# Optimization experiments

Hardware: AMD Instinct MI355X
Metric: run time of the kernel (lower is better)

The kernel has to match this reference:

```python
import jax, jax.numpy as jnp
import numpy as np
import math

B, S, HID = 1, 2048, 4096
NH, NKV, HD = 32, 8, 128
GROUPS = NH // NKV
THETA = 10000.0
NEG_INF = -1e9


def _ste(x, q):
    # straight-through estimator: forward uses q, backward passes grad to x
    return x + jax.lax.stop_gradient(q - x)


def fq_per_token(x):
    # symmetric int8 fake-quant, dynamic per-token scale over last dim
    s = jnp.maximum(jnp.max(jnp.abs(x), axis=-1, keepdims=True), 1e-8) / 127.0
    q = jnp.clip(jnp.round(x / s), -128.0, 127.0) * s
    return _ste(x, q)


def fq_per_channel(x):
    # symmetric int8 fake-quant, per-(head, channel) scale for K/V [B,H,S,D]
    s = jnp.maximum(jnp.max(jnp.abs(x), axis=(0, 2), keepdims=True), 1e-8) / 127.0
    q = jnp.clip(jnp.round(x / s), -128.0, 127.0) * s
    return _ste(x, q)


def _rotate_half(x):
    x1, x2 = jnp.split(x, 2, axis=-1)
    return jnp.concatenate([-x2, x1], axis=-1)


def _rope(position_ids):
    inv_freq = 1.0 / (THETA ** (jnp.arange(0, HD, 2, dtype=jnp.float32) / HD))
    freqs = position_ids.astype(jnp.float32)[..., None] * inv_freq  # [B,S,HD/2]
    emb = jnp.concatenate([freqs, freqs], axis=-1)                  # [B,S,HD]
    return jnp.cos(emb)[:, None, :, :], jnp.sin(emb)[:, None, :, :]


def setup_inputs() -> dict:
    key = jax.random.key(0)
    ks = jax.random.split(key, 9)
    w = 0.02
    return {
        "hidden_states": jax.random.normal(ks[0], (B, S, HID), dtype=jnp.float32),
        "position_ids": jnp.arange(B * S, dtype=jnp.int64 if jax.config.jax_enable_x64 else jnp.int32).reshape(B, S) % S,
        "Wq": jax.random.normal(ks[1], (HID, HID), dtype=jnp.float32) * w,
        "Wk": jax.random.normal(ks[2], (NKV * HD, HID), dtype=jnp.float32) * w,
        "Wv": jax.random.normal(ks[3], (NKV * HD, HID), dtype=jnp.float32) * w,
        "Wo": jax.random.normal(ks[4], (HID, HID), dtype=jnp.float32) * w,
        "qbias1": jax.random.normal(ks[5], (HID,), dtype=jnp.float32) * 0.01,
        "qbias2": jax.random.normal(ks[6], (HID,), dtype=jnp.float32) * 0.01,
        "o_scale2": jnp.ones((HID,), dtype=jnp.float32),
    }


def reference(hidden_states, position_ids, Wq, Wk, Wv, Wo, qbias1, qbias2, o_scale2):
    dtype = hidden_states.dtype
    # --- input activation quantization fused with qbias1 ---
    hs = fq_per_token(hidden_states - qbias1) + qbias1

    q = (hs @ Wq.T).reshape(B, S, NH, HD).transpose(0, 2, 1, 3)   # [B,NH,S,D]
    k = (hs @ Wk.T).reshape(B, S, NKV, HD).transpose(0, 2, 1, 3)  # [B,NKV,S,D]
    v = (hs @ Wv.T).reshape(B, S, NKV, HD).transpose(0, 2, 1, 3)

    cos, sin = _rope(position_ids)
    q = q * cos + _rotate_half(q) * sin
    k = k * cos + _rotate_half(k) * sin

    # repeat_kv for GQA
    k = jnp.repeat(k, GROUPS, axis=1)  # [B,NH,S,D]
    v = jnp.repeat(v, GROUPS, axis=1)

    # --- quantized QK^T ---
    k = fq_per_channel(k)          # qkt_matmul.quant_x2
    qq = fq_per_token(q)           # qkt_matmul quantizes x1
    attn = jnp.einsum("bhqd,bhkd->bhqk", qq, k) / math.sqrt(HD)

    # causal mask
    causal = jnp.tril(jnp.ones((S, S), dtype=bool))
    attn = jnp.where(causal[None, None], attn, jnp.asarray(NEG_INF, attn.dtype))

    attn = jax.nn.softmax(attn.astype(jnp.float32), axis=-1).astype(dtype)

    # --- quantized PV ---
    v = fq_per_channel(v)          # pv_matmul.quant_x2
    p = fq_per_token(attn)         # pv_matmul quantizes x1
    out = jnp.einsum("bhqk,bhkd->bhqd", p, v)
    out = fq_per_token(out)        # out_quant=True

    out = out.transpose(0, 2, 1, 3).reshape(B, S, HID)
    out = out * o_scale2
    # output activation quantization fused with qbias2
    out = fq_per_token(out - qbias2) + qbias2
    return out @ Wo.T
```

## Files before the change

kernel.cpp:

```cpp
#include <hip/hip_runtime.h>
#include <stdint.h>

typedef _Float16 f16;
typedef __bf16 bf16;
typedef f16 f16x4 __attribute__((ext_vector_type(4)));
typedef f16 f16x8 __attribute__((ext_vector_type(8)));
typedef bf16 bf16x4 __attribute__((ext_vector_type(4)));
typedef bf16 bf16x8 __attribute__((ext_vector_type(8)));
typedef float f32x4 __attribute__((ext_vector_type(4)));

#define SEQ 2048
#define HID 4096
#define NH 32
#define NKV 8
#define HD 128
#define NQKV 6144

__device__ __forceinline__ float fq_round(float x, float s){
  float r = rintf(x / s);
  r = fminf(fmaxf(r, -128.f), 127.f);
  return r * s;
}

__device__ __forceinline__ void gload_lds16(const void* g, void* l){
  __builtin_amdgcn_global_load_lds(
      (const __attribute__((address_space(1))) uint32_t*)g,
      (__attribute__((address_space(3))) uint32_t*)l, 16, 0, 0);
}

__device__ __forceinline__ void stage_g8(const void* gbase, size_t row_bytes, void* lds, int tid){
  int w = tid >> 6, l = tid & 63;
  #pragma unroll
  for (int i = 0; i < 4; i++){
    int flat = i * 256 + w * 64 + l;
    int r = flat >> 3, g = flat & 7;
    const char* src = (const char*)gbase + (size_t)r * row_bytes + (size_t)((g ^ (r & 7)) << 4);
    char* dst = (char*)lds + (size_t)(i * 256 + w * 64) * 16;
    gload_lds16(src, dst);
  }
}
__device__ __forceinline__ void stage_g16(const void* gbase, size_t row_bytes, void* lds, int tid){
  int w = tid >> 6, l = tid & 63;
  #pragma unroll
  for (int i = 0; i < 4; i++){
    int flat = i * 256 + w * 64 + l;
    int r = flat >> 4, g = flat & 15;
    const char* src = (const char*)gbase + (size_t)r * row_bytes + (size_t)((g ^ (r & 15)) << 4);
    char* dst = (char*)lds + (size_t)(i * 256 + w * 64) * 16;
    gload_lds16(src, dst);
  }
}

__global__ __launch_bounds__(256) void cvt_bf16_k(const float* __restrict__ x, bf16* __restrict__ y, int n4){
  int i = blockIdx.x * 256 + threadIdx.x;
  if (i < n4){
    float4 v = ((const float4*)x)[i];
    bf16x4 o = { (bf16)v.x, (bf16)v.y, (bf16)v.z, (bf16)v.w };
    ((bf16x4*)y)[i] = o;
  }
}

__global__ __launch_bounds__(256) void rope_table_k(const int* __restrict__ pos, float* __restrict__ cosT, float* __restrict__ sinT){
  int idx = blockIdx.x * 256 + threadIdx.x;
  int t = idx >> 6, j = idx & 63;
  float inv = powf(10000.f, -(float)j * (1.f/64.f));
  float f = (float)pos[t] * inv;
  cosT[idx] = cosf(f);
  sinT[idx] = sinf(f);
}

__global__ __launch_bounds__(256) void fq_hs_k(const float* __restrict__ h, const float* __restrict__ qb1, bf16* __restrict__ hs){
  int t = blockIdx.x, tid = threadIdx.x;
  const float* row = h + (size_t)t * HID;
  float x[16];
  float amax = 0.f;
  #pragma unroll
  for (int i = 0; i < 16; i++){
    int c = tid + i * 256;
    float v = row[c] - qb1[c];
    x[i] = v;
    amax = fmaxf(amax, fabsf(v));
  }
  #pragma unroll
  for (int d = 1; d < 64; d <<= 1) amax = fmaxf(amax, __shfl_xor(amax, d));
  __shared__ float red[4];
  if ((tid & 63) == 0) red[tid >> 6] = amax;
  __syncthreads();
  amax = fmaxf(fmaxf(red[0], red[1]), fmaxf(red[2], red[3]));
  float s = fmaxf(amax, 1e-8f) / 127.f;
  #pragma unroll
  for (int i = 0; i < 16; i++){
    int c = tid + i * 256;
    float q = fq_round(x[i], s) + qb1[c];
    hs[(size_t)t * HID + c] = (bf16)q;
  }
}

__global__ __launch_bounds__(512, 2) void gemm8(const bf16* __restrict__ A, const bf16* __restrict__ B,
                                                float* __restrict__ C, int N, int K){
  __shared__ bf16 As[2][256 * 64];
  __shared__ bf16 Bs[2][192 * 64];
  int orig = blockIdx.y * gridDim.x + blockIdx.x;
  int nid = (orig & 7) * 32 + (orig >> 3);
  int bm = (nid >> 5) * 256, bn = (nid & 31) * 192;
  int tid = threadIdx.x, lane = tid & 63, wid = tid >> 6;
  int wr = wid >> 2, wc = wid & 3;
  int lq = lane & 15, lg = lane >> 4;
  f32x4 acc[8][3] = {};
  int nk = K >> 6;

  const bf16* Abase = A + (size_t)bm * K;
  const bf16* Bbase = B + (size_t)bn * K;
  size_t rowb = (size_t)K * 2;

  auto stage_a = [&](bf16* lds, int t){
    const char* g0 = (const char*)Abase + (size_t)t * 128;
    #pragma unroll
    for (int i = 0; i < 4; i++){
      int f = i * 512 + tid;
      int r = f >> 3, g = f & 7;
      gload_lds16(g0 + (size_t)r * rowb + (size_t)((g ^ (r & 7)) << 4),
                  (char*)lds + (size_t)f * 16);
    }
  };
  auto stage_b = [&](bf16* lds, int t){
    const char* g0 = (const char*)Bbase + (size_t)t * 128;
    #pragma unroll
    for (int i = 0; i < 3; i++){
      int f = i * 512 + tid;
      int r = f >> 3, g = f & 7;
      gload_lds16(g0 + (size_t)r * rowb + (size_t)((g ^ (r & 7)) << 4),
                  (char*)lds + (size_t)f * 16);
    }
  };

  stage_a(As[0], 0);
  stage_b(Bs[0], 0);

  for (int t = 0; t < nk; t++){
    if (t + 1 < nk){
      stage_a(As[(t + 1) & 1], t + 1);
      stage_b(Bs[(t + 1) & 1], t + 1);
      asm volatile("s_waitcnt vmcnt(7)" ::: "memory");
    } else {
      asm volatile("s_waitcnt vmcnt(0)" ::: "memory");
    }
    __builtin_amdgcn_s_barrier();
    const bf16* at = As[t & 1];
    const bf16* bt = Bs[t & 1];

    bf16x8 bfr[3][2];
    #pragma unroll
    for (int nf = 0; nf < 3; nf++){
      int rr = wc * 48 + nf * 16 + lq;
      #pragma unroll
      for (int ks = 0; ks < 2; ks++){
        int gg = ks * 4 + lg;
        bfr[nf][ks] = *(const bf16x8*)(bt + rr * 64 + ((gg ^ (rr & 7)) << 3));
      }
    }
    #pragma unroll
    for (int mh = 0; mh < 2; mh++){
      bf16x8 af[4][2];
      #pragma unroll
      for (int mf = 0; mf < 4; mf++){
        int rr = wr * 128 + mh * 64 + mf * 16 + lq;
        #pragma unroll
        for (int ks = 0; ks < 2; ks++){
          int gg = ks * 4 + lg;
          af[mf][ks] = *(const bf16x8*)(at + rr * 64 + ((gg ^ (rr & 7)) << 3));
        }
      }
      __builtin_amdgcn_s_setprio(1);
      #pragma unroll
      for (int mf = 0; mf < 4; mf++)
        #pragma unroll
        for (int nf = 0; nf < 3; nf++)
          #pragma unroll
          for (int ks = 0; ks < 2; ks++)
            acc[mh * 4 + mf][nf] =
              __builtin_amdgcn_mfma_f32_16x16x32_bf16(af[mf][ks], bfr[nf][ks],
                                                      acc[mh * 4 + mf][nf], 0, 0, 0);
      __builtin_amdgcn_s_setprio(0);
    }
    __builtin_amdgcn_s_barrier();
  }

  #pragma unroll
  for (int mfg = 0; mfg < 8; mfg++){
    int mrow = bm + wr * 128 + mfg * 16 + 4 * lg;
    #pragma unroll
    for (int nfg = 0; nfg < 3; nfg++){
      int ncol = bn + wc * 48 + nfg * 16 + lq;
      #pragma unroll
      for (int i = 0; i < 4; i++)
        C[(size_t)(mrow + i) * N + ncol] = acc[mfg][nfg][i];
    }
  }
}

__global__ __launch_bounds__(256, 2) void gemm_bt(const bf16* __restrict__ A, const bf16* __restrict__ B,
                                                  float* __restrict__ C, int N, int K){
  __shared__ bf16 As[2][128 * 64];
  __shared__ bf16 Bs[2][128 * 64];
  int bm = blockIdx.y * 128, bn = blockIdx.x * 128;
  int tid = threadIdx.x, wid = tid >> 6, lane = tid & 63;
  int wr = wid >> 1, wc = wid & 1;
  f32x4 acc[4][4] = {};
  int nk = K >> 6;
  stage_g8(A + (size_t)bm * K, (size_t)K * 2, As[0], tid);
  stage_g8(B + (size_t)bn * K, (size_t)K * 2, Bs[0], tid);
  for (int t = 0; t < nk; t++){
    if (t + 1 < nk){
      stage_g8(A + (size_t)bm * K + (t + 1) * 64, (size_t)K * 2, As[(t + 1) & 1], tid);
      stage_g8(B + (size_t)bn * K + (t + 1) * 64, (size_t)K * 2, Bs[(t + 1) & 1], tid);
      asm volatile("s_waitcnt vmcnt(8)" ::: "memory");
    } else {
      asm volatile("s_waitcnt vmcnt(0)" ::: "memory");
    }
    __builtin_amdgcn_s_barrier();
    const bf16* at = As[t & 1];
    const bf16* bt = Bs[t & 1];
    __builtin_amdgcn_s_setprio(1);
    #pragma unroll
    for (int ks2 = 0; ks2 < 2; ks2++){
      bf16x8 af[4], bfr[4];
      int g = ks2 * 4 + (lane >> 4);
      #pragma unroll
      for (int mf = 0; mf < 4; mf++){
        int rr = wr * 64 + mf * 16 + (lane & 15);
        af[mf] = *(const bf16x8*)(at + rr * 64 + ((g ^ (rr & 7)) << 3));
      }
      #pragma unroll
      for (int nf = 0; nf < 4; nf++){
        int rr = wc * 64 + nf * 16 + (lane & 15);
        bfr[nf] = *(const bf16x8*)(bt + rr * 64 + ((g ^ (rr & 7)) << 3));
      }
      #pragma unroll
      for (int mf = 0; mf < 4; mf++)
        #pragma unroll
        for (int nf = 0; nf < 4; nf++)
          acc[mf][nf] = __builtin_amdgcn_mfma_f32_16x16x32_bf16(af[mf], bfr[nf], acc[mf][nf], 0, 0, 0);
    }
    __builtin_amdgcn_s_setprio(0);
    __builtin_amdgcn_s_barrier();
  }
  int mrow = bm + wr * 64 + 4 * (lane >> 4);
  int ncol = bn + wc * 64 + (lane & 15);
  #pragma unroll
  for (int mf = 0; mf < 4; mf++)
    #pragma unroll
    for (int nf = 0; nf < 4; nf++)
      #pragma unroll
      for (int i = 0; i < 4; i++)
        C[(size_t)(mrow + mf * 16 + i) * N + ncol + nf * 16] = acc[mf][nf][i];
}

__global__ __launch_bounds__(256) void rope_q_k(const float* __restrict__ qraw, const float* __restrict__ cosT,
                                                const float* __restrict__ sinT, f16* __restrict__ qf){
  int row = blockIdx.x * 4 + (threadIdx.x >> 6);
  int lane = threadIdx.x & 63;
  int hh = row >> 11, t = row & 2047;
  const float* qp = qraw + (size_t)t * NQKV + hh * HD;
  float q1 = qp[lane], q2 = qp[lane + 64];
  float c = cosT[t * 64 + lane], s = sinT[t * 64 + lane];
  float r1 = q1 * c - q2 * s;
  float r2 = q2 * c + q1 * s;
  float amax = fmaxf(fabsf(r1), fabsf(r2));
  #pragma unroll
  for (int d = 1; d < 64; d <<= 1) amax = fmaxf(amax, __shfl_xor(amax, d));
  float sc = fmaxf(amax, 1e-8f) / 127.f;
  const float kq = 0.08838834764831845f;
  f16* o = qf + ((size_t)hh * SEQ + t) * HD;
  o[lane]      = (f16)(fq_round(r1, sc) * kq);
  o[lane + 64] = (f16)(fq_round(r2, sc) * kq);
}

__global__ __launch_bounds__(256) void rope_k_k(const float* __restrict__ kraw, const float* __restrict__ cosT,
                                                const float* __restrict__ sinT, float* __restrict__ krope){
  int row = blockIdx.x * 4 + (threadIdx.x >> 6);
  int lane = threadIdx.x & 63;
  int kvh = row >> 11, t = row & 2047;
  const float* kp = kraw + (size_t)t * NQKV + 4096 + kvh * HD;
  float k1 = kp[lane], k2 = kp[lane + 64];
  float c = cosT[t * 64 + lane], s = sinT[t * 64 + lane];
  float* o = krope + ((size_t)kvh * SEQ + t) * HD;
  o[lane]      = k1 * c - k2 * s;
  o[lane + 64] = k2 * c + k1 * s;
}

__global__ __launch_bounds__(256) void kmax_part(const float* __restrict__ krope, float* __restrict__ kamax){
  int kvh = blockIdx.x >> 3, slice = blockIdx.x & 7;
  int c = threadIdx.x & 127, rh = threadIdx.x >> 7;
  const float* p = krope + ((size_t)kvh * SEQ + slice * 256 + rh) * HD + c;
  float a = 0.f;
  #pragma unroll 8
  for (int r = 0; r < 128; r++) a = fmaxf(a, fabsf(p[(size_t)r * 2 * HD]));
  atomicMax((int*)&kamax[kvh * 128 + c], __float_as_int(a));
}

__global__ __launch_bounds__(256) void vmax_part(const float* __restrict__ qkvraw, float* __restrict__ vamax){
  int slice = blockIdx.x;
  int tid = threadIdx.x;
  const float4* p = (const float4*)qkvraw;
  float a0 = 0.f, a1 = 0.f, a2 = 0.f, a3 = 0.f;
  for (int r = 0; r < 256; r++){
    float4 v = p[(size_t)(slice * 256 + r) * 1536 + 1280 + tid];
    a0 = fmaxf(a0, fabsf(v.x)); a1 = fmaxf(a1, fabsf(v.y));
    a2 = fmaxf(a2, fabsf(v.z)); a3 = fmaxf(a3, fabsf(v.w));
  }
  atomicMax((int*)&vamax[tid * 4 + 0], __float_as_int(a0));
  atomicMax((int*)&vamax[tid * 4 + 1], __float_as_int(a1));
  atomicMax((int*)&vamax[tid * 4 + 2], __float_as_int(a2));
  atomicMax((int*)&vamax[tid * 4 + 3], __float_as_int(a3));
}

__global__ __launch_bounds__(256) void quant_k_k(const float* __restrict__ krope, const float* __restrict__ kamax,
                                                 f16* __restrict__ kf){
  int idx = blockIdx.x * 256 + threadIdx.x;
  int d = idx & 127;
  int h = idx >> 18;
  float s = fmaxf(kamax[(h << 7) + d], 1e-8f) / 127.f;
  kf[idx] = (f16)fq_round(krope[idx], s);
}

__global__ __launch_bounds__(256) void quant_v_k(const float* __restrict__ qkvraw, const float* __restrict__ vamax,
                                                 f16* __restrict__ vt){
  __shared__ float tile[64][65];
  int t0 = blockIdx.x * 64;
  int c0 = blockIdx.y * 64;
  int tx = threadIdx.x & 63, ty = threadIdx.x >> 6;
  #pragma unroll
  for (int i = 0; i < 16; i++){
    int r = i * 4 + ty;
    tile[r][tx] = qkvraw[(size_t)(t0 + r) * NQKV + 5120 + c0 + tx];
  }
  __syncthreads();
  #pragma unroll
  for (int i = 0; i < 16; i++){
    int dch = i * 4 + ty;
    int ch = c0 + dch;
    float s = fmaxf(vamax[ch], 1e-8f) / 127.f;
    vt[(size_t)ch * SEQ + t0 + tx] = (f16)fq_round(tile[tx][dch], s);
  }
}

__global__ __launch_bounds__(256, 2) void attn_k(const f16* __restrict__ qf, const f16* __restrict__ kf,
                                                 const f16* __restrict__ vt, float* __restrict__ aout){
  int pr = blockIdx.x;
  int hh = blockIdx.y;
  int qtA = pr, qtB = 31 - pr;
  int kvh = hh >> 2;
  int tid = threadIdx.x, wid = tid >> 6, lane = tid & 63;
  int lq = lane & 15, lg = lane >> 4;

  __shared__ f16 ks[2][64 * 128];
  __shared__ f16 vs[2][128 * 64];
  __shared__ f16 ps[4][16][80];

  f16x8 bqA[4], bqB[4];
  {
    const f16* qbA = qf + ((size_t)hh * SEQ + qtA * 64 + wid * 16 + lq) * HD + lg * 8;
    const f16* qbB = qf + ((size_t)hh * SEQ + qtB * 64 + wid * 16 + lq) * HD + lg * 8;
    #pragma unroll
    for (int kk = 0; kk < 4; kk++){
      bqA[kk] = *(const f16x8*)(qbA + kk * 32);
      bqB[kk] = *(const f16x8*)(qbB + kk * 32);
    }
  }
  int qgA = qtA * 64 + wid * 16 + lq;
  int qgB = qtB * 64 + wid * 16 + lq;

  const f16* kbase = kf + (size_t)kvh * SEQ * HD;
  const f16* vbase = vt + (size_t)kvh * HD * SEQ;
  int nkb = qtB + 1;

  float mxA = -1e30f, mxB = -1e30f;
  stage_g16(kbase, (size_t)HD * 2, ks[0], tid);
  for (int kb = 0; kb < nkb; kb++){
    if (kb + 1 < nkb){
      stage_g16(kbase + (size_t)(kb + 1) * 64 * HD, (size_t)HD * 2, ks[(kb + 1) & 1], tid);
      asm volatile("s_waitcnt vmcnt(4)" ::: "memory");
    } else {
      asm volatile("s_waitcnt vmcnt(0)" ::: "memory");
    }
    __builtin_amdgcn_s_barrier();
    const f16* kt = ks[kb & 1];
    bool doA = (kb <= qtA);
    __builtin_amdgcn_s_setprio(1);
    #pragma unroll
    for (int nf = 0; nf < 4; nf++){
      int rr = nf * 16 + lq;
      f16x8 ka[4];
      #pragma unroll
      for (int kk = 0; kk < 4; kk++)
        ka[kk] = *(const f16x8*)(kt + rr * 128 + (((kk * 4 + lg) ^ (rr & 15)) << 3));
      int k0 = kb * 64 + nf * 16 + lg * 4;
      f32x4 sB = {0.f, 0.f, 0.f, 0.f};
      #pragma unroll
      for (int kk = 0; kk < 4; kk++) sB = __builtin_amdgcn_mfma_f32_16x16x32_f16(ka[kk], bqB[kk], sB, 0, 0, 0);
      #pragma unroll
      for (int i = 0; i < 4; i++)
        if (k0 + i <= qgB) mxB = fmaxf(mxB, sB[i]);
      if (doA){
        f32x4 sA = {0.f, 0.f, 0.f, 0.f};
        #pragma unroll
        for (int kk = 0; kk < 4; kk++) sA = __builtin_amdgcn_mfma_f32_16x16x32_f16(ka[kk], bqA[kk], sA, 0, 0, 0);
        #pragma unroll
        for (int i = 0; i < 4; i++)
          if (k0 + i <= qgA) mxA = fmaxf(mxA, sA[i]);
      }
    }
    __builtin_amdgcn_s_setprio(0);
    __builtin_amdgcn_s_barrier();
  }
  mxB = fmaxf(mxB, __shfl_xor(mxB, 16)); mxB = fmaxf(mxB, __shfl_xor(mxB, 32));
  mxA = fmaxf(mxA, __shfl_xor(mxA, 16)); mxA = fmaxf(mxA, __shfl_xor(mxA, 32));

  float lsA = 0.f, lsB = 0.f;
  f32x4 oA[8] = {}, oB[8] = {};
  stage_g16(kbase, (size_t)HD * 2, ks[0], tid);
  stage_g8(vbase, (size_t)SEQ * 2, vs[0], tid);
  for (int kb = 0; kb < nkb; kb++){
    if (kb + 1 < nkb){
      stage_g16(kbase + (size_t)(kb + 1) * 64 * HD, (size_t)HD * 2, ks[(kb + 1) & 1], tid);
      stage_g8(vbase + (kb + 1) * 64, (size_t)SEQ * 2, vs[(kb + 1) & 1], tid);
      asm volatile("s_waitcnt vmcnt(8)" ::: "memory");
    } else {
      asm volatile("s_waitcnt vmcnt(0)" ::: "memory");
    }
    __builtin_amdgcn_s_barrier();
    const f16* kt = ks[kb & 1];
    const f16* vtile = vs[kb & 1];
    bool doA = (kb <= qtA);
    f32x4 saccA[4];

    __builtin_amdgcn_s_setprio(1);
    #pragma unroll
    for (int nf = 0; nf < 4; nf++){
      int rr = nf * 16 + lq;
      f16x8 ka[4];
      #pragma unroll
      for (int kk = 0; kk < 4; kk++)
        ka[kk] = *(const f16x8*)(kt + rr * 128 + (((kk * 4 + lg) ^ (rr & 15)) << 3));
      f32x4 sB = {0.f, 0.f, 0.f, 0.f};
      #pragma unroll
      for (int kk = 0; kk < 4; kk++) sB = __builtin_amdgcn_mfma_f32_16x16x32_f16(ka[kk], bqB[kk], sB, 0, 0, 0);
      if (doA){
        f32x4 sA = {0.f, 0.f, 0.f, 0.f};
        #pragma unroll
        for (int kk = 0; kk < 4; kk++) sA = __builtin_amdgcn_mfma_f32_16x16x32_f16(ka[kk], bqA[kk], sA, 0, 0, 0);
        saccA[nf] = sA;
      }
      int k0 = kb * 64 + nf * 16 + lg * 4;
      f16x4 pB4;
      #pragma unroll
      for (int i = 0; i < 4; i++){
        float e = __expf(sB[i] - mxB);
        bool ok = (k0 + i <= qgB);
        lsB += ok ? e : 0.f;
        pB4[i] = (f16)(ok ? rintf(127.f * e) : 0.f);
      }
      *(f16x4*)&ps[wid][lq][nf * 16 + lg * 4] = pB4;
    }
    {
      f16x8 pa0 = *(const f16x8*)&ps[wid][lq][lg * 8];
      f16x8 pa1 = *(const f16x8*)&ps[wid][lq][32 + lg * 8];
      #pragma unroll
      for (int nf2 = 0; nf2 < 8; nf2++){
        int rr = nf2 * 16 + lq;
        f16x8 v0 = *(const f16x8*)(vtile + rr * 64 + (((lg) ^ (rr & 7)) << 3));
        f16x8 v1 = *(const f16x8*)(vtile + rr * 64 + (((4 + lg) ^ (rr & 7)) << 3));
        oB[nf2] = __builtin_amdgcn_mfma_f32_16x16x32_f16(pa0, v0, oB[nf2], 0, 0, 0);
        oB[nf2] = __builtin_amdgcn_mfma_f32_16x16x32_f16(pa1, v1, oB[nf2], 0, 0, 0);
      }
    }
    if (doA){
      #pragma unroll
      for (int nf = 0; nf < 4; nf++){
        int k0 = kb * 64 + nf * 16 + lg * 4;
        f16x4 pA4;
        #pragma unroll
        for (int i = 0; i < 4; i++){
          float e = __expf(saccA[nf][i] - mxA);
          bool ok = (k0 + i <= qgA);
          lsA += ok ? e : 0.f;
          pA4[i] = (f16)(ok ? rintf(127.f * e) : 0.f);
        }
        *(f16x4*)&ps[wid][lq][nf * 16 + lg * 4] = pA4;
      }
      f16x8 pa0 = *(const f16x8*)&ps[wid][lq][lg * 8];
      f16x8 pa1 = *(const f16x8*)&ps[wid][lq][32 + lg * 8];
      #pragma unroll
      for (int nf2 = 0; nf2 < 8; nf2++){
        int rr = nf2 * 16 + lq;
        f16x8 v0 = *(const f16x8*)(vtile + rr * 64 + (((lg) ^ (rr & 7)) << 3));
        f16x8 v1 = *(const f16x8*)(vtile + rr * 64 + (((4 + lg) ^ (rr & 7)) << 3));
        oA[nf2] = __builtin_amdgcn_mfma_f32_16x16x32_f16(pa0, v0, oA[nf2], 0, 0, 0);
        oA[nf2] = __builtin_amdgcn_mfma_f32_16x16x32_f16(pa1, v1, oA[nf2], 0, 0, 0);
      }
    }
    __builtin_amdgcn_s_setprio(0);
    __builtin_amdgcn_s_barrier();
  }

  lsB += __shfl_xor(lsB, 16); lsB += __shfl_xor(lsB, 32);
  lsA += __shfl_xor(lsA, 16); lsA += __shfl_xor(lsA, 32);

  auto epilogue = [&](f32x4* oacc, float lrow, int qt){
    float i127[4];
    #pragma unroll
    for (int i = 0; i < 4; i++)
      i127[i] = 1.f / (127.f * __shfl(lrow, lg * 4 + i));
    float am[4] = {0.f, 0.f, 0.f, 0.f};
    #pragma unroll
    for (int nf2 = 0; nf2 < 8; nf2++)
      #pragma unroll
      for (int i = 0; i < 4; i++)
        am[i] = fmaxf(am[i], fabsf(oacc[nf2][i] * i127[i]));
    #pragma unroll
    for (int i = 0; i < 4; i++){
      float a = am[i];
      #pragma unroll
      for (int d = 1; d < 16; d <<= 1) a = fmaxf(a, __shfl_xor(a, d));
      am[i] = a;
    }
    #pragma unroll
    for (int i = 0; i < 4; i++){
      float so = fmaxf(am[i], 1e-8f) / 127.f;
      int row = qt * 64 + wid * 16 + lg * 4 + i;
      float* op = aout + ((size_t)hh * SEQ + row) * HD + lq;
      #pragma unroll
      for (int nf2 = 0; nf2 < 8; nf2++){
        float v = oacc[nf2][i] * i127[i];
        op[nf2 * 16] = fq_round(v, so);
      }
    }
  };
  epilogue(oB, lsB, qtB);
  epilogue(oA, lsA, qtA);
}

__global__ __launch_bounds__(256) void epi_k(const float* __restrict__ aout, const float* __restrict__ osc,
                                             const float* __restrict__ qb2, bf16* __restrict__ act){
  int t = blockIdx.x, tid = threadIdx.x;
  float z[16]; float amax = 0.f;
  #pragma unroll
  for (int i = 0; i < 16; i++){
    int o = tid + i * 256;
    int h = o >> 7, d = o & 127;
    float y = aout[((size_t)h * SEQ + t) * HD + d] * osc[o];
    float zz = y - qb2[o];
    z[i] = zz;
    amax = fmaxf(amax, fabsf(zz));
  }
  #pragma unroll
  for (int d = 1; d < 64; d <<= 1) amax = fmaxf(amax, __shfl_xor(amax, d));
  __shared__ float red[4];
  if ((tid & 63) == 0) red[tid >> 6] = amax;
  __syncthreads();
  amax = fmaxf(fmaxf(red[0], red[1]), fmaxf(red[2], red[3]));
  float s = fmaxf(amax, 1e-8f) / 127.f;
  #pragma unroll
  for (int i = 0; i < 16; i++){
    int o = tid + i * 256;
    act[(size_t)t * HID + o] = (bf16)(fq_round(z[i], s) + qb2[o]);
  }
}

extern "C" void kernel_launch(void* const* d_in, const int* in_sizes, int n_in,
                              void* d_out, int out_size, void* d_ws, size_t ws_size,
                              hipStream_t stream) {
  const float* hidden = (const float*)d_in[0];
  const int*   pos    = (const int*)d_in[1];
  const float* Wq     = (const float*)d_in[2];
  const float* Wk     = (const float*)d_in[3];
  const float* Wv     = (const float*)d_in[4];
  const float* Wo     = (const float*)d_in[5];
  const float* qb1    = (const float*)d_in[6];
  const float* qb2    = (const float*)d_in[7];
  const float* osc    = (const float*)d_in[8];
  float* out = (float*)d_out;

  char* w = (char*)d_ws;
  size_t off = 0;
  auto take = [&](size_t b) -> char* {
    char* p = w + off;
    off += (b + 255) & ~(size_t)255;
    return p;
  };
  bf16* qkvW  = (bf16*)take((size_t)NQKV * HID * 2);
  bf16* WoB   = (bf16*)take((size_t)HID * HID * 2);
  bf16* hsB   = (bf16*)take((size_t)SEQ * HID * 2);
  float* cosT = (float*)take((size_t)SEQ * 64 * 4);
  float* sinT = (float*)take((size_t)SEQ * 64 * 4);
  float* qkv_raw = (float*)take((size_t)SEQ * NQKV * 4);
  float* krope = (float*)take((size_t)NKV * SEQ * HD * 4);
  f16* qf  = (f16*)take((size_t)NH * SEQ * HD * 2);
  f16* kf  = (f16*)take((size_t)NKV * SEQ * HD * 2);
  f16* vtf = (f16*)take((size_t)NKV * HD * SEQ * 2);
  float* kvamax = (float*)take(2048 * 4);
  float* kamax = kvamax, *vamax = kvamax + 1024;
  float* aout = qkv_raw;
  bf16*  act  = hsB;

  hipMemsetAsync(kvamax, 0, 2048 * sizeof(float), stream);
  cvt_bf16_k<<<16384, 256, 0, stream>>>(Wq, qkvW, 4194304);
  cvt_bf16_k<<<4096, 256, 0, stream>>>(Wk, qkvW + (size_t)4096 * HID, 1048576);
  cvt_bf16_k<<<4096, 256, 0, stream>>>(Wv, qkvW + (size_t)5120 * HID, 1048576);
  cvt_bf16_k<<<16384, 256, 0, stream>>>(Wo, WoB, 4194304);
  rope_table_k<<<512, 256, 0, stream>>>(pos, cosT, sinT);
  fq_hs_k<<<2048, 256, 0, stream>>>(hidden, qb1, hsB);
  gemm8<<<dim3(32, 8), 512, 0, stream>>>(hsB, qkvW, qkv_raw, NQKV, 4096);
  rope_q_k<<<16384, 256, 0, stream>>>(qkv_raw, cosT, sinT, qf);
  rope_k_k<<<4096, 256, 0, stream>>>(qkv_raw, cosT, sinT, krope);
  kmax_part<<<64, 256, 0, stream>>>(krope, kamax);
  vmax_part<<<8, 256, 0, stream>>>(qkv_raw, vamax);
  quant_k_k<<<8192, 256, 0, stream>>>(krope, kamax, kf);
  quant_v_k<<<dim3(32, 16), 256, 0, stream>>>(qkv_raw, vamax, vtf);
  attn_k<<<dim3(16, 32), 256, 0, stream>>>(qf, kf, vtf, aout);
  epi_k<<<2048, 256, 0, stream>>>(aout, osc, qb2, act);
  gemm_bt<<<dim3(32, 16), 256, 0, stream>>>(act, WoB, out, 4096, 4096);
}
```

Before: 448.5 us.

## Replace output projection GEMM with 256x128 tile, 512-thread kernel and tile remap

```diff
diff --git a/kernel.cpp b/kernel.cpp
--- a/kernel.cpp
+++ b/kernel.cpp
@@ -102,7 +102,7 @@
   __shared__ bf16 Bs[2][192 * 64];
   int orig = blockIdx.y * gridDim.x + blockIdx.x;
   int nid = (orig & 7) * 32 + (orig >> 3);
-  int bm = (nid >> 5) * 256, bn = (nid & 31) * 192;
+  int bm = (nid & 7) * 256, bn = (nid >> 3) * 192;
   int tid = threadIdx.x, lane = tid & 63, wid = tid >> 6;
   int wr = wid >> 2, wc = wid & 3;
   int lq = lane & 15, lg = lane >> 4;
@@ -199,61 +199,107 @@
   }
 }
 
-__global__ __launch_bounds__(256, 2) void gemm_bt(const bf16* __restrict__ A, const bf16* __restrict__ B,
-                                                  float* __restrict__ C, int N, int K){
-  __shared__ bf16 As[2][128 * 64];
+__global__ __launch_bounds__(512, 2) void gemm8o(const bf16* __restrict__ A, const bf16* __restrict__ B,
+                                                 float* __restrict__ C, int N, int K){
+  __shared__ bf16 As[2][256 * 64];
   __shared__ bf16 Bs[2][128 * 64];
-  int bm = blockIdx.y * 128, bn = blockIdx.x * 128;
-  int tid = threadIdx.x, wid = tid >> 6, lane = tid & 63;
-  int wr = wid >> 1, wc = wid & 1;
-  f32x4 acc[4][4] = {};
+  int orig = blockIdx.y * gridDim.x + blockIdx.x;
+  int nid = (orig & 7) * 32 + (orig >> 3);
+  int bm = (nid & 7) * 256, bn = (nid >> 3) * 128;
+  int tid = threadIdx.x, lane = tid & 63, wid = tid >> 6;
+  int wr = wid >> 2, wc = wid & 3;
+  int lq = lane & 15, lg = lane >> 4;
+  f32x4 acc[8][2] = {};
   int nk = K >> 6;
-  stage_g8(A + (size_t)bm * K, (size_t)K * 2, As[0], tid);
-  stage_g8(B + (size_t)bn * K, (size_t)K * 2, Bs[0], tid);
+
+  const bf16* Abase = A + (size_t)bm * K;
+  const bf16* Bbase = B + (size_t)bn * K;
+  size_t rowb = (size_t)K * 2;
+
+  auto stage_a = [&](bf16* lds, int t){
+    const char* g0 = (const char*)Abase + (size_t)t * 128;
+    #pragma unroll
+    for (int i = 0; i < 4; i++){
+      int f = i * 512 + tid;
+      int r = f >> 3, g = f & 7;
+      gload_lds16(g0 + (size_t)r * rowb + (size_t)((g ^ (r & 7)) << 4),
+                  (char*)lds + (size_t)f * 16);
+    }
+  };
+  auto stage_b = [&](bf16* lds, int t){
+    const char* g0 = (const char*)Bbase + (size_t)t * 128;
+    #pragma unroll
+    for (int i = 0; i < 2; i++){
+      int f = i * 512 + tid;
+      int r = f >> 3, g = f & 7;
+      gload_lds16(g0 + (size_t)r * rowb + (size_t)((g ^ (r & 7)) << 4),
+                  (char*)lds + (size_t)f * 16);
+    }
+  };
+
+  stage_a(As[0], 0);
+  stage_b(Bs[0], 0);
+
   for (int t = 0; t < nk; t++){
     if (t + 1 < nk){
-      stage_g8(A + (size_t)bm * K + (t + 1) * 64, (size_t)K * 2, As[(t + 1) & 1], tid);
-      stage_g8(B + (size_t)bn * K + (t + 1) * 64, (size_t)K * 2, Bs[(t + 1) & 1], tid);
-      asm volatile("s_waitcnt vmcnt(8)" ::: "memory");
+      stage_a(As[(t + 1) & 1], t + 1);
+      stage_b(Bs[(t + 1) & 1], t + 1);
+      asm volatile("s_waitcnt vmcnt(6)" ::: "memory");
     } else {
       asm volatile("s_waitcnt vmcnt(0)" ::: "memory");
     }
     __builtin_amdgcn_s_barrier();
     const bf16* at = As[t & 1];
     const bf16* bt = Bs[t & 1];
-    __builtin_amdgcn_s_setprio(1);
-    #pragma unroll
-    for (int ks2 = 0; ks2 < 2; ks2++){
-      bf16x8 af[4], bfr[4];
-      int g = ks2 * 4 + (lane >> 4);
+
+    bf16x8 bfr[2][2];
+    #pragma unroll
+    for (int nf = 0; nf < 2; nf++){
+      int rr = wc * 32 + nf * 16 + lq;
+      #pragma unroll
+      for (int ks = 0; ks < 2; ks++){
+        int gg = ks * 4 + lg;
+        bfr[nf][ks] = *(const bf16x8*)(bt + rr * 64 + ((gg ^ (rr & 7)) << 3));
+      }
+    }
+    #pragma unroll
+    for (int mh = 0; mh < 2; mh++){
+      bf16x8 af[4][2];
       #pragma unroll
       for (int mf = 0; mf < 4; mf++){
-        int rr = wr * 64 + mf * 16 + (lane & 15);
-        af[mf] = *(const bf16x8*)(at + rr * 64 + ((g ^ (rr & 7)) << 3));
-      }
-      #pragma unroll
-      for (int nf = 0; nf < 4; nf++){
-        int rr = wc * 64 + nf * 16 + (lane & 15);
-        bfr[nf] = *(const bf16x8*)(bt + rr * 64 + ((g ^ (rr & 7)) << 3));
-      }
+        int rr = wr * 128 + mh * 64 + mf * 16 + lq;
+        #pragma unroll
+        for (int ks = 0; ks < 2; ks++){
+          int gg = ks * 4 + lg;
+          af[mf][ks] = *(const bf16x8*)(at + rr * 64 + ((gg ^ (rr & 7)) << 3));
+        }
+      }
+      __builtin_amdgcn_s_setprio(1);
       #pragma unroll
       for (int mf = 0; mf < 4; mf++)
         #pragma unroll
-        for (int nf = 0; nf < 4; nf++)
-          acc[mf][nf] = __builtin_amdgcn_mfma_f32_16x16x32_bf16(af[mf], bfr[nf], acc[mf][nf], 0, 0, 0);
-    }
-    __builtin_amdgcn_s_setprio(0);
-    __builtin_amdgcn_s_barrier();
-  }
-  int mrow = bm + wr * 64 + 4 * (lane >> 4);
-  int ncol = bn + wc * 64 + (lane & 15);
-  #pragma unroll
-  for (int mf = 0; mf < 4; mf++)
-    #pragma unroll
-    for (int nf = 0; nf < 4; nf++)
+        for (int nf = 0; nf < 2; nf++)
+          #pragma unroll
+          for (int ks = 0; ks < 2; ks++)
+            acc[mh * 4 + mf][nf] =
+              __builtin_amdgcn_mfma_f32_16x16x32_bf16(af[mf][ks], bfr[nf][ks],
+                                                      acc[mh * 4 + mf][nf], 0, 0, 0);
+      __builtin_amdgcn_s_setprio(0);
+    }
+    __builtin_amdgcn_s_barrier();
+  }
+
+  #pragma unroll
+  for (int mfg = 0; mfg < 8; mfg++){
+    int mrow = bm + wr * 128 + mfg * 16 + 4 * lg;
+    #pragma unroll
+    for (int nfg = 0; nfg < 2; nfg++){
+      int ncol = bn + wc * 32 + nfg * 16 + lq;
       #pragma unroll
       for (int i = 0; i < 4; i++)
-        C[(size_t)(mrow + mf * 16 + i) * N + ncol + nf * 16] = acc[mf][nf][i];
+        C[(size_t)(mrow + i) * N + ncol] = acc[mfg][nfg][i];
+    }
+  }
 }
 
 __global__ __launch_bounds__(256) void rope_q_k(const float* __restrict__ qraw, const float* __restrict__ cosT,
@@ -620,5 +666,5 @@
   quant_v_k<<<dim3(32, 16), 256, 0, stream>>>(qkv_raw, vamax, vtf);
   attn_k<<<dim3(16, 32), 256, 0, stream>>>(qf, kf, vtf, aout);
   epi_k<<<2048, 256, 0, stream>>>(aout, osc, qb2, act);
-  gemm_bt<<<dim3(32, 16), 256, 0, stream>>>(act, WoB, out, 4096, 4096);
-}
+  gemm8o<<<dim3(32, 8), 512, 0, stream>>>(act, WoB, out, 4096, 4096);
+}
```

New measurement: 461.4 us. +2.9%, slower.

## Templatize 256-row GEMM, reuse it for output projection, reorder per-k-slice MFMA

Applied to the files above, without the earlier changes.

```diff
diff --git a/kernel.cpp b/kernel.cpp
--- a/kernel.cpp
+++ b/kernel.cpp
@@ -96,17 +96,18 @@
   }
 }
 
-__global__ __launch_bounds__(512, 2) void gemm8(const bf16* __restrict__ A, const bf16* __restrict__ B,
-                                                float* __restrict__ C, int N, int K){
+template<int NF>
+__global__ __launch_bounds__(512, 2) void gemm8p(const bf16* __restrict__ A, const bf16* __restrict__ B,
+                                                 float* __restrict__ C, int N, int K){
   __shared__ bf16 As[2][256 * 64];
-  __shared__ bf16 Bs[2][192 * 64];
+  __shared__ bf16 Bs[2][NF * 64 * 64];
   int orig = blockIdx.y * gridDim.x + blockIdx.x;
   int nid = (orig & 7) * 32 + (orig >> 3);
-  int bm = (nid >> 5) * 256, bn = (nid & 31) * 192;
+  int bm = (nid & 7) * 256, bn = (nid >> 3) * (NF * 64);
   int tid = threadIdx.x, lane = tid & 63, wid = tid >> 6;
   int wr = wid >> 2, wc = wid & 3;
   int lq = lane & 15, lg = lane >> 4;
-  f32x4 acc[8][3] = {};
+  f32x4 acc[8][NF] = {};
   int nk = K >> 6;
 
   const bf16* Abase = A + (size_t)bm * K;
@@ -126,7 +127,7 @@
   auto stage_b = [&](bf16* lds, int t){
     const char* g0 = (const char*)Bbase + (size_t)t * 128;
     #pragma unroll
-    for (int i = 0; i < 3; i++){
+    for (int i = 0; i < NF; i++){
       int f = i * 512 + tid;
       int r = f >> 3, g = f & 7;
       gload_lds16(g0 + (size_t)r * rowb + (size_t)((g ^ (r & 7)) << 4),
@@ -141,7 +142,8 @@
     if (t + 1 < nk){
       stage_a(As[(t + 1) & 1], t + 1);
       stage_b(Bs[(t + 1) & 1], t + 1);
-      asm volatile("s_waitcnt vmcnt(7)" ::: "memory");
+      if constexpr (NF == 3) asm volatile("s_waitcnt vmcnt(7)" ::: "memory");
+      else                   asm volatile("s_waitcnt vmcnt(6)" ::: "memory");
     } else {
       asm volatile("s_waitcnt vmcnt(0)" ::: "memory");
     }
@@ -149,111 +151,52 @@
     const bf16* at = As[t & 1];
     const bf16* bt = Bs[t & 1];
 
-    bf16x8 bfr[3][2];
-    #pragma unroll
-    for (int nf = 0; nf < 3; nf++){
-      int rr = wc * 48 + nf * 16 + lq;
-      #pragma unroll
-      for (int ks = 0; ks < 2; ks++){
-        int gg = ks * 4 + lg;
-        bfr[nf][ks] = *(const bf16x8*)(bt + rr * 64 + ((gg ^ (rr & 7)) << 3));
-      }
-    }
-    #pragma unroll
-    for (int mh = 0; mh < 2; mh++){
-      bf16x8 af[4][2];
-      #pragma unroll
-      for (int mf = 0; mf < 4; mf++){
-        int rr = wr * 128 + mh * 64 + mf * 16 + lq;
+    #pragma unroll
+    for (int ks = 0; ks < 2; ks++){
+      bf16x8 bfr[NF];
+      #pragma unroll
+      for (int mh = 0; mh < 2; mh++){
+        if (mh == 0){
+          #pragma unroll
+          for (int nf = 0; nf < NF; nf++){
+            int rr = wc * (NF * 16) + nf * 16 + lq;
+            int gg = ks * 4 + lg;
+            bfr[nf] = *(const bf16x8*)(bt + rr * 64 + ((gg ^ (rr & 7)) << 3));
+          }
+        }
+        bf16x8 af[4];
         #pragma unroll
-        for (int ks = 0; ks < 2; ks++){
+        for (int mf = 0; mf < 4; mf++){
+          int rr = wr * 128 + mh * 64 + mf * 16 + lq;
           int gg = ks * 4 + lg;
-          af[mf][ks] = *(const bf16x8*)(at + rr * 64 + ((gg ^ (rr & 7)) << 3));
+          af[mf] = *(const bf16x8*)(at + rr * 64 + ((gg ^ (rr & 7)) << 3));
         }
-      }
-      __builtin_amdgcn_s_setprio(1);
-      #pragma unroll
-      for (int mf = 0; mf < 4; mf++)
+        __builtin_amdgcn_s_barrier();
+        __builtin_amdgcn_s_setprio(1);
         #pragma unroll
-        for (int nf = 0; nf < 3; nf++)
+        for (int mf = 0; mf < 4; mf++)
           #pragma unroll
-          for (int ks = 0; ks < 2; ks++)
+          for (int nf = 0; nf < NF; nf++)
             acc[mh * 4 + mf][nf] =
-              __builtin_amdgcn_mfma_f32_16x16x32_bf16(af[mf][ks], bfr[nf][ks],
+              __builtin_amdgcn_mfma_f32_16x16x32_bf16(af[mf], bfr[nf],
                                                       acc[mh * 4 + mf][nf], 0, 0, 0);
-      __builtin_amdgcn_s_setprio(0);
-    }
-    __builtin_amdgcn_s_barrier();
+        __builtin_amdgcn_s_setprio(0);
+        __builtin_amdgcn_s_barrier();
+      }
+    }
   }
 
   #pragma unroll
   for (int mfg = 0; mfg < 8; mfg++){
     int mrow = bm + wr * 128 + mfg * 16 + 4 * lg;
     #pragma unroll
-    for (int nfg = 0; nfg < 3; nfg++){
-      int ncol = bn + wc * 48 + nfg * 16 + lq;
+    for (int nfg = 0; nfg < NF; nfg++){
+      int ncol = bn + wc * (NF * 16) + nfg * 16 + lq;
       #pragma unroll
       for (int i = 0; i < 4; i++)
         C[(size_t)(mrow + i) * N + ncol] = acc[mfg][nfg][i];
     }
   }
-}
-
-__global__ __launch_bounds__(256, 2) void gemm_bt(const bf16* __restrict__ A, const bf16* __restrict__ B,
-                                                  float* __restrict__ C, int N, int K){
-  __shared__ bf16 As[2][128 * 64];
-  __shared__ bf16 Bs[2][128 * 64];
-  int bm = blockIdx.y * 128, bn = blockIdx.x * 128;
-  int tid = threadIdx.x, wid = tid >> 6, lane = tid & 63;
-  int wr = wid >> 1, wc = wid & 1;
-  f32x4 acc[4][4] = {};
-  int nk = K >> 6;
-  stage_g8(A + (size_t)bm * K, (size_t)K * 2, As[0], tid);
-  stage_g8(B + (size_t)bn * K, (size_t)K * 2, Bs[0], tid);
-  for (int t = 0; t < nk; t++){
-    if (t + 1 < nk){
-      stage_g8(A + (size_t)bm * K + (t + 1) * 64, (size_t)K * 2, As[(t + 1) & 1], tid);
-      stage_g8(B + (size_t)bn * K + (t + 1) * 64, (size_t)K * 2, Bs[(t + 1) & 1], tid);
-      asm volatile("s_waitcnt vmcnt(8)" ::: "memory");
-    } else {
-      asm volatile("s_waitcnt vmcnt(0)" ::: "memory");
-    }
-    __builtin_amdgcn_s_barrier();
-    const bf16* at = As[t & 1];
-    const bf16* bt = Bs[t & 1];
-    __builtin_amdgcn_s_setprio(1);
-    #pragma unroll
-    for (int ks2 = 0; ks2 < 2; ks2++){
-      bf16x8 af[4], bfr[4];
-      int g = ks2 * 4 + (lane >> 4);
-      #pragma unroll
-      for (int mf = 0; mf < 4; mf++){
-        int rr = wr * 64 + mf * 16 + (lane & 15);
-        af[mf] = *(const bf16x8*)(at + rr * 64 + ((g ^ (rr & 7)) << 3));
-      }
-      #pragma unroll
-      for (int nf = 0; nf < 4; nf++){
-        int rr = wc * 64 + nf * 16 + (lane & 15);
-        bfr[nf] = *(const bf16x8*)(bt + rr * 64 + ((g ^ (rr & 7)) << 3));
-      }
-      #pragma unroll
-      for (int mf = 0; mf < 4; mf++)
-        #pragma unroll
-        for (int nf = 0; nf < 4; nf++)
-          acc[mf][nf] = __builtin_amdgcn_mfma_f32_16x16x32_bf16(af[mf], bfr[nf], acc[mf][nf], 0, 0, 0);
-    }
-    __builtin_amdgcn_s_setprio(0);
-    __builtin_amdgcn_s_barrier();
-  }
-  int mrow = bm + wr * 64 + 4 * (lane >> 4);
-  int ncol = bn + wc * 64 + (lane & 15);
-  #pragma unroll
-  for (int mf = 0; mf < 4; mf++)
-    #pragma unroll
-    for (int nf = 0; nf < 4; nf++)
-      #pragma unroll
-      for (int i = 0; i < 4; i++)
-        C[(size_t)(mrow + mf * 16 + i) * N + ncol + nf * 16] = acc[mf][nf][i];
 }
 
 __global__ __launch_bounds__(256) void rope_q_k(const float* __restrict__ qraw, const float* __restrict__ cosT,
@@ -611,7 +554,7 @@
   cvt_bf16_k<<<16384, 256, 0, stream>>>(Wo, WoB, 4194304);
   rope_table_k<<<512, 256, 0, stream>>>(pos, cosT, sinT);
   fq_hs_k<<<2048, 256, 0, stream>>>(hidden, qb1, hsB);
-  gemm8<<<dim3(32, 8), 512, 0, stream>>>(hsB, qkvW, qkv_raw, NQKV, 4096);
+  gemm8p<3><<<dim3(32, 8), 512, 0, stream>>>(hsB, qkvW, qkv_raw, NQKV, 4096);
   rope_q_k<<<16384, 256, 0, stream>>>(qkv_raw, cosT, sinT, qf);
   rope_k_k<<<4096, 256, 0, stream>>>(qkv_raw, cosT, sinT, krope);
   kmax_part<<<64, 256, 0, stream>>>(krope, kamax);
@@ -620,5 +563,5 @@
   quant_v_k<<<dim3(32, 16), 256, 0, stream>>>(qkv_raw, vamax, vtf);
   attn_k<<<dim3(16, 32), 256, 0, stream>>>(qf, kf, vtf, aout);
   epi_k<<<2048, 256, 0, stream>>>(aout, osc, qb2, act);
-  gemm_bt<<<dim3(32, 16), 256, 0, stream>>>(act, WoB, out, 4096, 4096);
-}
+  gemm8p<2><<<dim3(32, 8), 512, 0, stream>>>(act, WoB, out, 4096, 4096);
+}
```

Measured after the change: 488.2 us. +8.9%, slower.
